# Kernel tuning notes

Hardware: AMD Instinct MI355X
Metric: run time of the kernel (lower is better)

Reference implementation:

```python
import jax, jax.numpy as jnp
import numpy as np

NEG = -1e6  # SequenceMask fill value from original code


def setup_inputs() -> dict:
    key = jax.random.key(0)
    ks = jax.random.split(key, 7)
    B, Tq, Tk, U = 32, 1024, 1024, 256
    return {
        "query": jax.random.normal(ks[0], (B, Tq, U), dtype=jnp.float32),
        "key": jax.random.normal(ks[1], (B, Tk, U), dtype=jnp.float32),
        "value": jax.random.normal(ks[2], (B, Tk, U), dtype=jnp.float32),
        "valid_length": jax.random.randint(ks[3], (B,), 0, Tk, dtype=jnp.int32),
        "W_k": jax.random.normal(ks[4], (U, U), dtype=jnp.float32) * (1.0 / np.sqrt(U)),
        "W_q": jax.random.normal(ks[5], (U, U), dtype=jnp.float32) * (1.0 / np.sqrt(U)),
        "v": jax.random.normal(ks[6], (U,), dtype=jnp.float32) * (1.0 / np.sqrt(U)),
    }


def reference(query, key, value, valid_length, W_k, W_q, v):
    # Original applies W_k to query and W_q to key (naming swap kept faithfully).
    tq = jnp.tanh(jnp.einsum('bqu,vu->bqv', query, W_k))  # (B,Tq,U)
    tk = jnp.tanh(jnp.einsum('bku,vu->bkv', key, W_q))    # (B,Tk,U)
    # v is linear over (tq_i + tk_j): decompose to avoid (B,Tq,Tk,U) tensor.
    sq = jnp.einsum('bqu,u->bq', tq, v)  # (B,Tq)
    sk = jnp.einsum('bku,u->bk', tk, v)  # (B,Tk)
    scores = sq[:, :, None] + sk[:, None, :]  # (B,Tq,Tk)
    Tk_ = key.shape[1]
    mask = jnp.arange(Tk_)[None, None, :] < valid_length[:, None, None]  # (B,1,Tk)
    scores = jnp.where(mask, scores, NEG)
    attn = jax.nn.softmax(scores, axis=-1)  # dropout p=0 (eval) -> identity
    return jnp.einsum('bqk,bkd->bqd', attn, value)
```

## Files before the change

### kernel.cpp

```cpp
#include <hip/hip_runtime.h>
#include <hip/hip_fp16.h>
#include <math.h>

#define NB 32
#define TQ 1024
#define TK 1024
#define UD 256

typedef __attribute__((ext_vector_type(8))) _Float16 f16x8;
typedef __attribute__((ext_vector_type(4))) _Float16 f16x4;
typedef __attribute__((ext_vector_type(4))) float f32x4;

__device__ __forceinline__ float fast_tanh(float x) {
  const float e = __expf(2.0f * x);
  return 1.0f - 2.0f / (e + 1.0f);
}

__global__ __launch_bounds__(256) void cvt_wq_kernel(
    const float* __restrict__ Wq, _Float16* __restrict__ wq16t) {
  const int idx = blockIdx.x * 256 + threadIdx.x;
  const int u = idx >> 5;
  const int ks = idx & 31;
  const float4 w0 = *reinterpret_cast<const float4*>(Wq + u * UD + ks * 8);
  const float4 w1 = *reinterpret_cast<const float4*>(Wq + u * UD + ks * 8 + 4);
  f16x8 h;
  h[0] = (_Float16)w0.x; h[1] = (_Float16)w0.y;
  h[2] = (_Float16)w0.z; h[3] = (_Float16)w0.w;
  h[4] = (_Float16)w1.x; h[5] = (_Float16)w1.y;
  h[6] = (_Float16)w1.z; h[7] = (_Float16)w1.w;
  *reinterpret_cast<f16x8*>(wq16t + ((size_t)ks * 256 + u) * 8) = h;
}

__global__ __launch_bounds__(512, 4) void sk_mfma_kernel(
    const float* __restrict__ key, const _Float16* __restrict__ wq16t,
    const float* __restrict__ v, float* __restrict__ sk) {
  __shared__ _Float16 At[32 * 64 * 8];
  __shared__ _Float16 Bt[2][4 * 256 * 8];

  const int tid = threadIdx.x;
  const int lane = tid & 63;
  const int wid = tid >> 6;
  const int wr = wid >> 2;
  const int wc = wid & 3;
  const int lx = lane & 15;
  const int lg = lane >> 4;
  const int row0 = blockIdx.x * 64;

  float4 areg[8];
#pragma unroll
  for (int i = 0; i < 8; ++i) {
    const int r = wid * 8 + i;
    areg[i] = *reinterpret_cast<const float4*>(key + (size_t)(row0 + r) * UD +
                                               lane * 4);
  }
  f16x8 b0a = reinterpret_cast<const f16x8*>(wq16t)[tid];
  f16x8 b0b = reinterpret_cast<const f16x8*>(wq16t)[tid + 512];

  {
    const int ks = lane >> 1;
    const int jh = lane & 1;
#pragma unroll
    for (int i = 0; i < 8; ++i) {
      const int r = wid * 8 + i;
      f16x4 h;
      h[0] = (_Float16)areg[i].x; h[1] = (_Float16)areg[i].y;
      h[2] = (_Float16)areg[i].z; h[3] = (_Float16)areg[i].w;
      const int rs = r ^ (ks & 7);
      *reinterpret_cast<f16x4*>(At + ((ks * 64 + rs) * 8 + jh * 4)) = h;
    }
  }
  reinterpret_cast<f16x8*>(Bt[0])[tid] = b0a;
  reinterpret_cast<f16x8*>(Bt[0])[tid + 512] = b0b;
  __syncthreads();

  f32x4 acc[2][4];
#pragma unroll
  for (int m = 0; m < 2; ++m)
#pragma unroll
    for (int n = 0; n < 4; ++n) acc[m][n] = (f32x4){0.f, 0.f, 0.f, 0.f};

#pragma unroll
  for (int p = 0; p < 8; ++p) {
    const int cur = p & 1;
    f16x8 breg0, breg1;
    if (p < 7) {
      const f16x8* src =
          reinterpret_cast<const f16x8*>(wq16t + (size_t)(p + 1) * 8192);
      breg0 = src[tid];
      breg1 = src[tid + 512];
    }
    const int ksg = p * 4 + lg;
    f16x8 af[2], bf[4];
#pragma unroll
    for (int m = 0; m < 2; ++m) {
      const int row = wr * 32 + m * 16 + lx;
      const int rs = row ^ (ksg & 7);
      af[m] = *reinterpret_cast<const f16x8*>(At + (ksg * 64 + rs) * 8);
    }
#pragma unroll
    for (int n = 0; n < 4; ++n) {
      const int u = wc * 64 + n * 16 + lx;
      bf[n] = *reinterpret_cast<const f16x8*>(Bt[cur] + (lg * 256 + u) * 8);
    }
#pragma unroll
    for (int m = 0; m < 2; ++m)
#pragma unroll
      for (int n = 0; n < 4; ++n)
        acc[m][n] = __builtin_amdgcn_mfma_f32_16x16x32_f16(af[m], bf[n],
                                                           acc[m][n], 0, 0, 0);
    if (p < 7) {
      reinterpret_cast<f16x8*>(Bt[cur ^ 1])[tid] = breg0;
      reinterpret_cast<f16x8*>(Bt[cur ^ 1])[tid + 512] = breg1;
    }
    __syncthreads();
  }

  float vv[4];
#pragma unroll
  for (int n = 0; n < 4; ++n) vv[n] = v[wc * 64 + n * 16 + lx];

  float* red = (float*)At;
  float part[2][4];
#pragma unroll
  for (int m = 0; m < 2; ++m)
#pragma unroll
    for (int r = 0; r < 4; ++r) part[m][r] = 0.f;
#pragma unroll
  for (int m = 0; m < 2; ++m)
#pragma unroll
    for (int n = 0; n < 4; ++n)
#pragma unroll
      for (int r = 0; r < 4; ++r)
        part[m][r] += vv[n] * fast_tanh(acc[m][n][r]);

#pragma unroll
  for (int m = 0; m < 2; ++m)
#pragma unroll
    for (int r = 0; r < 4; ++r) {
      float s = part[m][r];
      s += __shfl_xor(s, 1);
      s += __shfl_xor(s, 2);
      s += __shfl_xor(s, 4);
      s += __shfl_xor(s, 8);
      if (lx == 0) red[(wr * 32 + m * 16 + lg * 4 + r) * 4 + wc] = s;
    }
  __syncthreads();
  if (tid < 64) {
    sk[row0 + tid] = red[tid * 4 + 0] + red[tid * 4 + 1] + red[tid * 4 + 2] +
                     red[tid * 4 + 3];
  }
}

__global__ __launch_bounds__(256) void pv_kernel(
    const float* __restrict__ sk, const int* __restrict__ vlen,
    const float* __restrict__ value, float* __restrict__ part) {
  const int b = blockIdx.x >> 4;
  const int ch = blockIdx.x & 15;
  const int tid = threadIdx.x;
  const int vl = vlen[b];
  __shared__ float wbuf[64];
  __shared__ float red4[8];
  const float* skb = sk + b * TK;

  if (vl == 0) {
    if (tid < 64) wbuf[tid] = 1.0f / (float)TK;
  } else {
    float m = -1e30f;
#pragma unroll
    for (int idx = 0; idx < 4; ++idx) {
      const int k = tid + idx * 256;
      if (k < vl) m = fmaxf(m, skb[k]);
    }
    for (int off = 1; off < 64; off <<= 1) m = fmaxf(m, __shfl_xor(m, off));
    if ((tid & 63) == 0) red4[tid >> 6] = m;
    __syncthreads();
    m = fmaxf(fmaxf(red4[0], red4[1]), fmaxf(red4[2], red4[3]));
    float zs = 0.f;
#pragma unroll
    for (int idx = 0; idx < 4; ++idx) {
      const int k = tid + idx * 256;
      zs += (k < vl) ? __expf(skb[k] - m) : 0.f;
    }
    for (int off = 1; off < 64; off <<= 1) zs += __shfl_xor(zs, off);
    if ((tid & 63) == 0) red4[4 + (tid >> 6)] = zs;
    __syncthreads();
    const float rz = 1.0f / (red4[4] + red4[5] + red4[6] + red4[7]);
    if (tid < 64) {
      const int k = ch * 64 + tid;
      wbuf[tid] = (k < vl) ? __expf(skb[k] - m) * rz : 0.f;
    }
  }
  __syncthreads();

  const int d = tid;
  const float* vb = value + ((size_t)b * TK + ch * 64) * UD;
  float acc = 0.f;
#pragma unroll 8
  for (int k = 0; k < 64; ++k)
    acc = fmaf(wbuf[k], vb[(size_t)k * UD + d], acc);
  part[(size_t)(b * 16 + ch) * UD + d] = acc;
}

__global__ __launch_bounds__(256) void bcast_kernel(
    const float* __restrict__ part, float* __restrict__ out) {
  const int b = blockIdx.x >> 4;
  const int qc = blockIdx.x & 15;
  const int tid = threadIdx.x;
  const int qoff = tid >> 6;
  const int dd = (tid & 63) * 4;

  float4 s = make_float4(0.f, 0.f, 0.f, 0.f);
#pragma unroll
  for (int c = 0; c < 16; ++c) {
    const float4 p = *reinterpret_cast<const float4*>(
        &part[(size_t)(b * 16 + c) * UD + dd]);
    s.x += p.x; s.y += p.y; s.z += p.z; s.w += p.w;
  }

  float* ob = out + (size_t)b * TQ * UD + (size_t)qc * 64 * UD;
#pragma unroll 4
  for (int q4 = 0; q4 < 16; ++q4) {
    *reinterpret_cast<float4*>(&ob[(size_t)(q4 * 4 + qoff) * UD + dd]) = s;
  }
}

extern "C" void kernel_launch(void* const* d_in, const int* in_sizes, int n_in,
                              void* d_out, int out_size, void* d_ws,
                              size_t ws_size, hipStream_t stream) {
  const float* key = (const float*)d_in[1];
  const float* value = (const float*)d_in[2];
  const int* vlen = (const int*)d_in[3];
  const float* Wq = (const float*)d_in[5];
  const float* v = (const float*)d_in[6];
  float* out = (float*)d_out;

  char* ws = (char*)d_ws;
  _Float16* wq16t = (_Float16*)(ws);
  float* sk = (float*)(ws + 131072);
  float* part = (float*)(ws + 262144);

  cvt_wq_kernel<<<32, 256, 0, stream>>>(Wq, wq16t);
  sk_mfma_kernel<<<(NB * TK) / 64, 512, 0, stream>>>(key, wq16t, v, sk);
  pv_kernel<<<NB * 16, 256, 0, stream>>>(sk, vlen, value, part);
  bcast_kernel<<<NB * 16, 256, 0, stream>>>(part, out);
}
```

Measured before the change: 49.01 us.

## Fuse score projection with value weighting and defer softmax normalization

The key-score MFMA kernel and the value-weighting kernel are merged into one. Each block turns its 64 scores directly into unnormalized exponentials, accumulates the weighted value rows for that chunk, and writes a per-chunk partition sum. The broadcast kernel now adds up the partition sums and applies the normalization. This removes a kernel launch, the score round trip through global memory, and the redundant per-block max/sum passes over all keys. The cost is that the max subtraction is dropped, which relies on scores being bounded (sum of |v| times tanh) to avoid exp overflow.

```diff
diff --git a/kernel.cpp b/kernel.cpp
--- a/kernel.cpp
+++ b/kernel.cpp
@@ -31,11 +31,14 @@
   *reinterpret_cast<f16x8*>(wq16t + ((size_t)ks * 256 + u) * 8) = h;
 }
 
-__global__ __launch_bounds__(512, 4) void sk_mfma_kernel(
+__global__ __launch_bounds__(512, 4) void fused_kernel(
     const float* __restrict__ key, const _Float16* __restrict__ wq16t,
-    const float* __restrict__ v, float* __restrict__ sk) {
+    const float* __restrict__ v, const int* __restrict__ vlen,
+    const float* __restrict__ value, float* __restrict__ part,
+    float* __restrict__ zpart) {
   __shared__ _Float16 At[32 * 64 * 8];
   __shared__ _Float16 Bt[2][4 * 256 * 8];
+  __shared__ float wbuf[64];
 
   const int tid = threadIdx.x;
   const int lane = tid & 63;
@@ -45,6 +48,8 @@
   const int lx = lane & 15;
   const int lg = lane >> 4;
   const int row0 = blockIdx.x * 64;
+  const int b = blockIdx.x >> 4;
+  const int ch = blockIdx.x & 15;
 
   float4 areg[8];
 #pragma unroll
@@ -120,24 +125,24 @@
   for (int n = 0; n < 4; ++n) vv[n] = v[wc * 64 + n * 16 + lx];
 
   float* red = (float*)At;
-  float part[2][4];
-#pragma unroll
-  for (int m = 0; m < 2; ++m)
-#pragma unroll
-    for (int r = 0; r < 4; ++r) part[m][r] = 0.f;
+  float prt[2][4];
+#pragma unroll
+  for (int m = 0; m < 2; ++m)
+#pragma unroll
+    for (int r = 0; r < 4; ++r) prt[m][r] = 0.f;
 #pragma unroll
   for (int m = 0; m < 2; ++m)
 #pragma unroll
     for (int n = 0; n < 4; ++n)
 #pragma unroll
       for (int r = 0; r < 4; ++r)
-        part[m][r] += vv[n] * fast_tanh(acc[m][n][r]);
+        prt[m][r] += vv[n] * fast_tanh(acc[m][n][r]);
 
 #pragma unroll
   for (int m = 0; m < 2; ++m)
 #pragma unroll
     for (int r = 0; r < 4; ++r) {
-      float s = part[m][r];
+      float s = prt[m][r];
       s += __shfl_xor(s, 1);
       s += __shfl_xor(s, 2);
       s += __shfl_xor(s, 4);
@@ -145,70 +150,54 @@
       if (lx == 0) red[(wr * 32 + m * 16 + lg * 4 + r) * 4 + wc] = s;
     }
   __syncthreads();
+
+  const int vl = vlen[b];
   if (tid < 64) {
-    sk[row0 + tid] = red[tid * 4 + 0] + red[tid * 4 + 1] + red[tid * 4 + 2] +
-                     red[tid * 4 + 3];
-  }
-}
-
-__global__ __launch_bounds__(256) void pv_kernel(
-    const float* __restrict__ sk, const int* __restrict__ vlen,
-    const float* __restrict__ value, float* __restrict__ part) {
-  const int b = blockIdx.x >> 4;
-  const int ch = blockIdx.x & 15;
-  const int tid = threadIdx.x;
-  const int vl = vlen[b];
-  __shared__ float wbuf[64];
-  __shared__ float red4[8];
-  const float* skb = sk + b * TK;
-
-  if (vl == 0) {
-    if (tid < 64) wbuf[tid] = 1.0f / (float)TK;
-  } else {
-    float m = -1e30f;
-#pragma unroll
-    for (int idx = 0; idx < 4; ++idx) {
-      const int k = tid + idx * 256;
-      if (k < vl) m = fmaxf(m, skb[k]);
-    }
-    for (int off = 1; off < 64; off <<= 1) m = fmaxf(m, __shfl_xor(m, off));
-    if ((tid & 63) == 0) red4[tid >> 6] = m;
-    __syncthreads();
-    m = fmaxf(fmaxf(red4[0], red4[1]), fmaxf(red4[2], red4[3]));
-    float zs = 0.f;
-#pragma unroll
-    for (int idx = 0; idx < 4; ++idx) {
-      const int k = tid + idx * 256;
-      zs += (k < vl) ? __expf(skb[k] - m) : 0.f;
-    }
-    for (int off = 1; off < 64; off <<= 1) zs += __shfl_xor(zs, off);
-    if ((tid & 63) == 0) red4[4 + (tid >> 6)] = zs;
-    __syncthreads();
-    const float rz = 1.0f / (red4[4] + red4[5] + red4[6] + red4[7]);
-    if (tid < 64) {
-      const int k = ch * 64 + tid;
-      wbuf[tid] = (k < vl) ? __expf(skb[k] - m) * rz : 0.f;
-    }
-  }
-  __syncthreads();
-
-  const int d = tid;
-  const float* vb = value + ((size_t)b * TK + ch * 64) * UD;
-  float acc = 0.f;
+    const float sval =
+        red[tid * 4 + 0] + red[tid * 4 + 1] + red[tid * 4 + 2] + red[tid * 4 + 3];
+    const int kglob = ch * 64 + tid;
+    const float e = (vl == 0) ? 1.0f : ((kglob < vl) ? __expf(sval) : 0.0f);
+    wbuf[tid] = e;
+    float zz = e;
+    zz += __shfl_xor(zz, 1);
+    zz += __shfl_xor(zz, 2);
+    zz += __shfl_xor(zz, 4);
+    zz += __shfl_xor(zz, 8);
+    zz += __shfl_xor(zz, 16);
+    zz += __shfl_xor(zz, 32);
+    if (tid == 0) zpart[b * 16 + ch] = zz;
+  }
+  __syncthreads();
+
+  const int half = tid >> 8;
+  const int d = tid & 255;
+  const float* vb =
+      value + ((size_t)b * TK + ch * 64 + half * 32) * UD + d;
+  float a = 0.f;
 #pragma unroll 8
-  for (int k = 0; k < 64; ++k)
-    acc = fmaf(wbuf[k], vb[(size_t)k * UD + d], acc);
-  part[(size_t)(b * 16 + ch) * UD + d] = acc;
+  for (int k = 0; k < 32; ++k)
+    a = fmaf(wbuf[half * 32 + k], vb[(size_t)k * UD], a);
+  float* racc = (float*)Bt;
+  racc[half * 256 + d] = a;
+  __syncthreads();
+  if (tid < 256)
+    part[(size_t)(b * 16 + ch) * UD + tid] = racc[tid] + racc[256 + tid];
 }
 
 __global__ __launch_bounds__(256) void bcast_kernel(
-    const float* __restrict__ part, float* __restrict__ out) {
+    const float* __restrict__ part, const float* __restrict__ zpart,
+    float* __restrict__ out) {
   const int b = blockIdx.x >> 4;
   const int qc = blockIdx.x & 15;
   const int tid = threadIdx.x;
   const int qoff = tid >> 6;
   const int dd = (tid & 63) * 4;
 
+  float Z = 0.f;
+#pragma unroll
+  for (int c = 0; c < 16; ++c) Z += zpart[b * 16 + c];
+  const float rz = 1.0f / Z;
+
   float4 s = make_float4(0.f, 0.f, 0.f, 0.f);
 #pragma unroll
   for (int c = 0; c < 16; ++c) {
@@ -216,6 +205,7 @@
         &part[(size_t)(b * 16 + c) * UD + dd]);
     s.x += p.x; s.y += p.y; s.z += p.z; s.w += p.w;
   }
+  s.x *= rz; s.y *= rz; s.z *= rz; s.w *= rz;
 
   float* ob = out + (size_t)b * TQ * UD + (size_t)qc * 64 * UD;
 #pragma unroll 4
@@ -236,11 +226,11 @@
 
   char* ws = (char*)d_ws;
   _Float16* wq16t = (_Float16*)(ws);
-  float* sk = (float*)(ws + 131072);
-  float* part = (float*)(ws + 262144);
+  float* part = (float*)(ws + 131072);
+  float* zpart = (float*)(ws + 655360);
 
   cvt_wq_kernel<<<32, 256, 0, stream>>>(Wq, wq16t);
-  sk_mfma_kernel<<<(NB * TK) / 64, 512, 0, stream>>>(key, wq16t, v, sk);
-  pv_kernel<<<NB * 16, 256, 0, stream>>>(sk, vlen, value, part);
-  bcast_kernel<<<NB * 16, 256, 0, stream>>>(part, out);
-}
+  fused_kernel<<<NB * 16, 512, 0, stream>>>(key, wq16t, v, vlen, value, part,
+                                            zpart);
+  bcast_kernel<<<NB * 16, 256, 0, stream>>>(part, zpart, out);
+}
```

Measured after the change: 44.91 us. -8.4%, faster.
